# Kernel optimization log

Hardware: AMD Instinct MI355X
Metric: run time of the kernel (lower is better)

The kernel has to match this reference:

```python
import jax, jax.numpy as jnp
import numpy as np
import math

DIM = 512
HEADS = 8
DH = DIM // HEADS
B, C, H, W = 2, 512, 48, 48


def setup_inputs() -> dict:
    key = jax.random.key(0)
    k1, k2, k3, k4 = jax.random.split(key, 4)
    x = jax.random.normal(k1, (B, C, H, W), dtype=jnp.float32)
    # torch Linear weights: [out_features, in_features]
    w_qkv = jax.random.normal(k2, (3 * DIM, DIM), dtype=jnp.float32) * (DIM ** -0.5)
    w_out = jax.random.normal(k3, (DIM, DIM), dtype=jnp.float32) * (DIM ** -0.5)
    b_out = jax.random.normal(k4, (DIM,), dtype=jnp.float32) * 0.01
    wavelength = jnp.asarray(0.1, dtype=jnp.float32)
    return {"x": x, "w_qkv": w_qkv, "w_out": w_out, "b_out": b_out, "wavelength": wavelength}


def reference(x, w_qkv, w_out, b_out, wavelength):
    b, c, h, w = x.shape
    n = h * w
    scale = DH ** -0.5

    x_flat = x.reshape(b, c, n).transpose(0, 2, 1)  # [B, N, C]
    qkv = jnp.einsum('bnc,dc->bnd', x_flat, w_qkv)   # [B, N, 3*DIM]
    q, k, v = jnp.split(qkv, 3, axis=-1)

    def to_heads(t):
        return t.reshape(b, n, HEADS, DH).transpose(0, 2, 1, 3)  # [B, h, N, dh]

    q, k, v = to_heads(q), to_heads(k), to_heads(v)

    dots = jnp.einsum('bhid,bhjd->bhij', q, k) * scale  # [B, h, N, N]

    # Fresnel interference bias over spatial positions
    yy, xx = jnp.meshgrid(jnp.arange(h), jnp.arange(w), indexing='ij')
    positions = jnp.stack([yy, xx], axis=-1).astype(jnp.float32).reshape(-1, 2)  # [N, 2]
    pos_diff = positions[None, :, :] - positions[:, None, :]  # [N, N, 2]
    distances = jnp.sqrt(jnp.sum(pos_diff ** 2, axis=-1) + 1e-8)  # [N, N]
    phase = 2.0 * math.pi * distances / (jnp.abs(wavelength) * h + 1e-6)
    interference = jnp.cos(phase)

    dots = dots + interference[None, None, :, :] * 0.1
    attn = jax.nn.softmax(dots, axis=-1)
    out = jnp.einsum('bhij,bhjd->bhid', attn, v)  # [B, h, N, dh]
    out = out.transpose(0, 2, 1, 3).reshape(b, n, HEADS * DH)  # [B, N, DIM]
    out = jnp.einsum('bnd,od->bno', out, w_out) + b_out
    return out.transpose(0, 2, 1).reshape(b, c, h, w)
```

## Files before the change

### kernel.cpp

```cpp
#include <hip/hip_runtime.h>
#include <math.h>

#define BB 2
#define CC 512
#define NN 2304
#define NH 8
#define DD 512
#define D3 1536
#define WIDTH 48
#define C1 0.18033688f

#define KSPLIT 3
#define KTILES 12
#define NTBL 213

typedef _Float16 h8 __attribute__((ext_vector_type(8)));
typedef _Float16 h4 __attribute__((ext_vector_type(4)));
typedef _Float16 h2 __attribute__((ext_vector_type(2)));
typedef float f4 __attribute__((ext_vector_type(4)));

__device__ __forceinline__ void gload16(const void* g, void* s) {
  __builtin_amdgcn_global_load_lds(
      (const __attribute__((address_space(1))) unsigned int*)g,
      (__attribute__((address_space(3))) unsigned int*)s, 16, 0, 0);
}

__global__ __launch_bounds__(256) void prep_k(
    const float* __restrict__ x, const float* __restrict__ wq,
    const float* __restrict__ wo, const float* __restrict__ wavp,
    _Float16* __restrict__ xt, _Float16* __restrict__ wqh,
    _Float16* __restrict__ woh, _Float16* __restrict__ btf)
{
  __shared__ float Ls[32][33];
  const int t = threadIdx.x;
  const int e = blockIdx.x;

  if (e < 2304) {
    const int n0 = (e % 72) * 32;
    const int c0 = ((e / 72) % 16) * 32;
    const int b  = e / 1152;
#pragma unroll
    for (int p = 0; p < 4; ++p) {
      const int cl = (t >> 5) + p * 8, nl = t & 31;
      Ls[cl][nl] = x[((size_t)b * CC + c0 + cl) * NN + n0 + nl];
    }
    __syncthreads();
#pragma unroll
    for (int p = 0; p < 2; ++p) {
      const int nl = (t >> 4) + p * 16, cl = (t & 15) * 2;
      h2 v = {(_Float16)Ls[cl][nl], (_Float16)Ls[cl + 1][nl]};
      *(h2*)(xt + ((size_t)b * NN + n0 + nl) * CC + c0 + cl) = v;
    }
  } else if (e < 3328) {
    const int idx = (e - 2304) * 256 + t;
    const int NQ = (D3 * CC) / 4;
    if (idx < NQ) {
      float4 v = *(const float4*)(wq + (size_t)idx * 4);
      h4 o = {(_Float16)v.x, (_Float16)v.y, (_Float16)v.z, (_Float16)v.w};
      *(h4*)(wqh + (size_t)idx * 4) = o;
    } else {
      const int j = idx - NQ;
      float4 v = *(const float4*)(wo + (size_t)j * 4);
      h4 o = {(_Float16)v.x, (_Float16)v.y, (_Float16)v.z, (_Float16)v.w};
      *(h4*)(woh + (size_t)j * 4) = o;
    }
  } else {
    const int tbl = (e - 3328) * 2 + (t >> 7);
    if (tbl < NTBL) {
      const int tid = t & 127;
      const int dD = tbl / 3, qm = tbl % 3;
      const int qt0 = qm + 36;
      const int kt0 = qt0 - (dD - 35);
      const int w = tid >> 6, quad = (tid >> 4) & 3, l15 = tid & 15;
      const float pc = 6.283185307179586f / (fabsf(wavp[0]) * (float)WIDTH + 1e-6f);
      _Float16* o = btf + ((size_t)tbl * 128 + tid) * 32;
#pragma unroll
      for (int g = 0; g < 4; ++g) {
        h8 v;
#pragma unroll
        for (int el = 0; el < 8; ++el) {
          const int j = g * 8 + el;
          const int nt = j >> 4, mt = (j >> 2) & 3, r = j & 3;
          const int q = qt0 * 64 + w * 32 + nt * 16 + l15;
          const int k = kt0 * 64 + mt * 16 + quad * 4 + r;
          const float dy = (float)(q / WIDTH) - (float)(k / WIDTH);
          const float dx = (float)(q % WIDTH) - (float)(k % WIDTH);
          const float dist = sqrtf(dy * dy + dx * dx + 1e-8f);
          v[el] = (_Float16)(0.1f * __cosf(dist * pc) * 1.44269504f);
        }
        *(h8*)(o + g * 8) = v;
      }
    }
  }
}

__global__ __launch_bounds__(256) void qkv_gemm_k(
    const _Float16* __restrict__ xt, const _Float16* __restrict__ wqh,
    _Float16* __restrict__ qb, _Float16* __restrict__ kb,
    _Float16* __restrict__ vb)
{
  __shared__ _Float16 Xs[128][32];
  __shared__ _Float16 Ws[128][32];
  const int t = threadIdx.x;
  const int lane = t & 63, w = t >> 6;
  const int l15 = lane & 15, quad = lane >> 4;
  const int wm = w & 1, wn = w >> 1;
  const int n0 = blockIdx.x * 128;
  const int d0 = blockIdx.y * 128;
  const int b  = blockIdx.z;
  const bool isv = (d0 >= 2 * DD);
  const _Float16* xb = xt + (size_t)b * NN * CC;

  const int srow = lane >> 2, scol = (lane & 3) * 8;

  f4 acc[4][4];
#pragma unroll
  for (int mt = 0; mt < 4; ++mt)
#pragma unroll
    for (int nt = 0; nt < 4; ++nt) acc[mt][nt] = (f4)(0.f);

  for (int c0 = 0; c0 < CC; c0 += 32) {
#pragma unroll
    for (int r = 0; r < 2; ++r) {
      const int ci = w + r * 4;
      const int row = ci * 16 + srow;
      gload16(xb + (size_t)(n0 + row) * CC + c0 + scol, &Xs[0][0] + ci * 512);
      gload16(wqh + (size_t)(d0 + row) * CC + c0 + scol, &Ws[0][0] + ci * 512);
    }
    __syncthreads();

    h8 wfr[4], xfr[4];
#pragma unroll
    for (int mt = 0; mt < 4; ++mt)
      wfr[mt] = *(const h8*)&Ws[wm * 64 + mt * 16 + l15][quad * 8];
#pragma unroll
    for (int nt = 0; nt < 4; ++nt)
      xfr[nt] = *(const h8*)&Xs[wn * 64 + nt * 16 + l15][quad * 8];

    if (!isv) {
#pragma unroll
      for (int mt = 0; mt < 4; ++mt)
#pragma unroll
        for (int nt = 0; nt < 4; ++nt)
          acc[mt][nt] = __builtin_amdgcn_mfma_f32_16x16x32_f16(
              wfr[mt], xfr[nt], acc[mt][nt], 0, 0, 0);
    } else {
#pragma unroll
      for (int mt = 0; mt < 4; ++mt)
#pragma unroll
        for (int nt = 0; nt < 4; ++nt)
          acc[mt][nt] = __builtin_amdgcn_mfma_f32_16x16x32_f16(
              xfr[nt], wfr[mt], acc[mt][nt], 0, 0, 0);
    }
    __syncthreads();
  }

  if (!isv) {
    const int which = d0 >> 9;
    _Float16* buf = which == 0 ? qb : kb;
    const int h = ((d0 & 511) >> 6) + wm;
#pragma unroll
    for (int mt = 0; mt < 4; ++mt) {
      const int dh = mt * 16 + quad * 4;
#pragma unroll
      for (int nt = 0; nt < 4; ++nt) {
        const int token = n0 + wn * 64 + nt * 16 + l15;
        h4 o = {(_Float16)acc[mt][nt][0], (_Float16)acc[mt][nt][1],
                (_Float16)acc[mt][nt][2], (_Float16)acc[mt][nt][3]};
        *(h4*)(buf + (((size_t)b * NH + h) * NN + token) * 64 + dh) = o;
      }
    }
  } else {
    const int h = ((d0 - 2 * DD) >> 6) + wm;
#pragma unroll
    for (int mt = 0; mt < 4; ++mt) {
      const int dh = mt * 16 + l15;
#pragma unroll
      for (int nt = 0; nt < 4; ++nt) {
        const int token = n0 + wn * 64 + nt * 16 + quad * 4;
        h4 o = {(_Float16)acc[mt][nt][0], (_Float16)acc[mt][nt][1],
                (_Float16)acc[mt][nt][2], (_Float16)acc[mt][nt][3]};
        *(h4*)(vb + (((size_t)b * NH + h) * 64 + dh) * NN + token) = o;
      }
    }
  }
}

__global__ __launch_bounds__(128, 4) void attn_k(
    const _Float16* __restrict__ qb, const _Float16* __restrict__ kb,
    const _Float16* __restrict__ vb, const _Float16* __restrict__ btf,
    _Float16* __restrict__ op, float* __restrict__ lp)
{
  __shared__ _Float16 Ks[64][72];
  __shared__ _Float16 Vs[64][72];

  const int t    = threadIdx.x;
  const int lane = t & 63;
  const int w    = t >> 6;
  const int l15  = lane & 15;
  const int quad = lane >> 4;
  const int qtile = blockIdx.x / KSPLIT;
  const int kq    = blockIdx.x % KSPLIT;
  const int n0 = qtile * 64;
  const int h  = blockIdx.y;
  const int b  = blockIdx.z;
  const size_t base = ((size_t)b * NH + h) * NN * 64;
  const _Float16* qp = qb + base;
  const _Float16* kp = kb + base;
  const _Float16* vp = vb + base;

  h8 qf[2][2];
#pragma unroll
  for (int nt = 0; nt < 2; ++nt)
#pragma unroll
    for (int ks = 0; ks < 2; ++ks)
      qf[nt][ks] = *(const h8*)(qp + (size_t)(n0 + w * 32 + nt * 16 + l15) * 64 +
                                ks * 32 + quad * 8);

  f4 oc[4][2];
#pragma unroll
  for (int mt = 0; mt < 4; ++mt)
#pragma unroll
    for (int nt = 0; nt < 2; ++nt) oc[mt][nt] = (f4)(0.f);
  float lac[2][2] = {};

  const int ktg0 = kq * KTILES;
  const _Float16* bp =
      btf + ((size_t)((qtile - ktg0 + 35) * 3 + qtile % 3) * 128 + t) * 32;

  for (int kt = 0; kt < KTILES; ++kt) {
    const int k0 = (ktg0 + kt) * 64;
    h8 kr[4], vr[4], bfr[4];
#pragma unroll
    for (int r = 0; r < 4; ++r) {
      const int c = t + r * 128;
      const int row = c >> 3, off = (c & 7) * 8;
      kr[r] = *(const h8*)(kp + (size_t)(k0 + row) * 64 + off);
      vr[r] = *(const h8*)(vp + (size_t)row * NN + k0 + off);
      bfr[r] = *(const h8*)(bp + r * 8);
    }
    bp -= 3 * 128 * 32;
    __syncthreads();
#pragma unroll
    for (int r = 0; r < 4; ++r) {
      const int c = t + r * 128;
      const int row = c >> 3, off = (c & 7) * 8;
      *(h8*)&Ks[row][off] = kr[r];
      *(h8*)&Vs[row][off] = vr[r];
    }
    __syncthreads();

    f4 st[4][2];
#pragma unroll
    for (int mt = 0; mt < 4; ++mt)
#pragma unroll
      for (int nt = 0; nt < 2; ++nt) st[mt][nt] = (f4)(0.f);
#pragma unroll
    for (int ks = 0; ks < 2; ++ks) {
#pragma unroll
      for (int mt = 0; mt < 4; ++mt) {
        h8 kf = *(const h8*)&Ks[mt * 16 + l15][ks * 32 + quad * 8];
#pragma unroll
        for (int nt = 0; nt < 2; ++nt)
          st[mt][nt] = __builtin_amdgcn_mfma_f32_16x16x32_f16(
              kf, qf[nt][ks], st[mt][nt], 0, 0, 0);
      }
    }

    __syncthreads();

#pragma unroll
    for (int nt = 0; nt < 2; ++nt) {
      const int q = w * 32 + nt * 16 + l15;
#pragma unroll
      for (int mt = 0; mt < 4; ++mt) {
        const int jb = nt * 16 + mt * 4;
        const float b0 = (float)bfr[jb >> 3][(jb & 7) + 0];
        const float b1 = (float)bfr[jb >> 3][(jb & 7) + 1];
        const float b2 = (float)bfr[jb >> 3][(jb & 7) + 2];
        const float b3 = (float)bfr[jb >> 3][(jb & 7) + 3];
        const float p0 = __builtin_exp2f(st[mt][nt][0] * C1 + b0);
        const float p1 = __builtin_exp2f(st[mt][nt][1] * C1 + b1);
        const float p2 = __builtin_exp2f(st[mt][nt][2] * C1 + b2);
        const float p3 = __builtin_exp2f(st[mt][nt][3] * C1 + b3);
        lac[nt][0] += p0 + p1;
        lac[nt][1] += p2 + p3;
        const auto plo = __builtin_amdgcn_cvt_pkrtz(p0, p1);
        const auto phi = __builtin_amdgcn_cvt_pkrtz(p2, p3);
        h4 pk = {(_Float16)plo[0], (_Float16)plo[1],
                 (_Float16)phi[0], (_Float16)phi[1]};
        *(h4*)&Ks[q][mt * 16 + quad * 4] = pk;
      }
    }

#pragma unroll
    for (int ks = 0; ks < 2; ++ks) {
      h8 pf[2];
#pragma unroll
      for (int nt = 0; nt < 2; ++nt)
        pf[nt] = *(const h8*)&Ks[w * 32 + nt * 16 + l15][ks * 32 + quad * 8];
#pragma unroll
      for (int mt = 0; mt < 4; ++mt) {
        h8 vf = *(const h8*)&Vs[mt * 16 + l15][ks * 32 + quad * 8];
#pragma unroll
        for (int nt = 0; nt < 2; ++nt)
          oc[mt][nt] = __builtin_amdgcn_mfma_f32_16x16x32_f16(
              vf, pf[nt], oc[mt][nt], 0, 0, 0);
      }
    }
  }

#pragma unroll
  for (int nt = 0; nt < 2; ++nt) {
    float l = lac[nt][0] + lac[nt][1];
    l += __shfl_xor(l, 16);
    l += __shfl_xor(l, 32);
    const float inv = 1.f / l;
    const int qi = n0 + w * 32 + nt * 16 + l15;
    _Float16* od = op + (size_t)kq * BB * NN * DD +
                   ((size_t)b * NN + qi) * DD + h * 64;
#pragma unroll
    for (int mt = 0; mt < 4; ++mt) {
      const int dh = mt * 16 + quad * 4;
      h4 o = {(_Float16)(oc[mt][nt][0] * inv), (_Float16)(oc[mt][nt][1] * inv),
              (_Float16)(oc[mt][nt][2] * inv), (_Float16)(oc[mt][nt][3] * inv)};
      *(h4*)(od + dh) = o;
    }
    if (quad == 0)
      lp[(size_t)kq * BB * NH * NN + ((size_t)b * NH + h) * NN + qi] = l;
  }
}

__global__ __launch_bounds__(256) void comb_k(
    const _Float16* __restrict__ op, const float* __restrict__ lp,
    _Float16* __restrict__ ho)
{
  const int idx = blockIdx.x * 256 + threadIdx.x;
  const int d8 = idx & 63;
  const int bn = idx >> 6;
  const int n = bn % NN, b = bn / NN;
  const int h = d8 >> 3;
  const size_t SL = (size_t)BB * NH * NN;
  const size_t SO = (size_t)BB * NN * DD;
  const size_t li = ((size_t)b * NH + h) * NN + n;
  const float l0 = lp[li];
  const float l1 = lp[SL + li];
  const float l2 = lp[2 * SL + li];
  const float inv = 1.f / (l0 + l1 + l2);
  const float w0 = l0 * inv, w1 = l1 * inv, w2 = l2 * inv;
  h8 o0 = *(const h8*)(op + (size_t)bn * DD + d8 * 8);
  h8 o1 = *(const h8*)(op + SO + (size_t)bn * DD + d8 * 8);
  h8 o2 = *(const h8*)(op + 2 * SO + (size_t)bn * DD + d8 * 8);
  h8 r;
#pragma unroll
  for (int i = 0; i < 8; ++i)
    r[i] = (_Float16)((float)o0[i] * w0 + (float)o1[i] * w1 + (float)o2[i] * w2);
  *(h8*)(ho + (size_t)bn * DD + d8 * 8) = r;
}

__global__ __launch_bounds__(64) void out_gemm_k(
    const _Float16* __restrict__ ho, const _Float16* __restrict__ woh,
    const float* __restrict__ bias, float* __restrict__ out)
{
  __shared__ _Float16 Hs[64][32];
  __shared__ _Float16 Ws2[64][32];
  const int t = threadIdx.x;
  const int l15 = t & 15, quad = t >> 4;
  const int n0 = blockIdx.x * 64;
  const int o0 = blockIdx.y * 64;
  const int b  = blockIdx.z;
  const int srow = t >> 2, scol = (t & 3) * 8;

  f4 acc[4][4];
#pragma unroll
  for (int mt = 0; mt < 4; ++mt)
#pragma unroll
    for (int nt = 0; nt < 4; ++nt) acc[mt][nt] = (f4)(0.f);

  for (int c0 = 0; c0 < DD; c0 += 32) {
#pragma unroll
    for (int ci = 0; ci < 4; ++ci) {
      const int row = ci * 16 + srow;
      gload16(ho + ((size_t)b * NN + n0 + row) * DD + c0 + scol,
              &Hs[0][0] + ci * 512);
      gload16(woh + (size_t)(o0 + row) * DD + c0 + scol,
              &Ws2[0][0] + ci * 512);
    }
    __syncthreads();
    h8 hf[4], wf[4];
#pragma unroll
    for (int mt = 0; mt < 4; ++mt)
      hf[mt] = *(const h8*)&Hs[mt * 16 + l15][quad * 8];
#pragma unroll
    for (int nt = 0; nt < 4; ++nt)
      wf[nt] = *(const h8*)&Ws2[nt * 16 + l15][quad * 8];
#pragma unroll
    for (int mt = 0; mt < 4; ++mt)
#pragma unroll
      for (int nt = 0; nt < 4; ++nt)
        acc[mt][nt] = __builtin_amdgcn_mfma_f32_16x16x32_f16(
            hf[mt], wf[nt], acc[mt][nt], 0, 0, 0);
    __syncthreads();
  }

#pragma unroll
  for (int nt = 0; nt < 4; ++nt) {
    const int o = o0 + nt * 16 + l15;
    const float bv = bias[o];
#pragma unroll
    for (int mt = 0; mt < 4; ++mt) {
      const int token = n0 + mt * 16 + quad * 4;
      float4 v = {acc[mt][nt][0] + bv, acc[mt][nt][1] + bv,
                  acc[mt][nt][2] + bv, acc[mt][nt][3] + bv};
      *(float4*)(out + ((size_t)b * DD + o) * NN + token) = v;
    }
  }
}

extern "C" void kernel_launch(void* const* d_in, const int* in_sizes, int n_in,
                              void* d_out, int out_size, void* d_ws, size_t ws_size,
                              hipStream_t stream)
{
  (void)in_sizes; (void)n_in; (void)out_size; (void)ws_size;
  const float* x     = (const float*)d_in[0];
  const float* w_qkv = (const float*)d_in[1];
  const float* w_out = (const float*)d_in[2];
  const float* b_out = (const float*)d_in[3];
  const float* wav   = (const float*)d_in[4];
  float* out = (float*)d_out;

  const size_t SZ  = (size_t)BB * NH * NN * 64;
  const size_t BTF = (size_t)NTBL * 128 * 32;

  _Float16* qb  = (_Float16*)d_ws;
  _Float16* kb  = qb + SZ;
  _Float16* vb  = kb + SZ;
  _Float16* btf = vb + SZ;
  _Float16* op  = btf + BTF;
  float*    lpf = (float*)(op + 3 * SZ);
  _Float16* woh = (_Float16*)(lpf + 3 * (size_t)BB * NH * NN);
  _Float16* ho  = qb;
  _Float16* xt  = op;
  _Float16* wqh = op + SZ;

  prep_k    <<<dim3(2304 + 1024 + 107), 256, 0, stream>>>(x, w_qkv, w_out, wav,
                                                          xt, wqh, woh, btf);
  qkv_gemm_k<<<dim3(NN / 128, D3 / 128, BB), 256, 0, stream>>>(xt, wqh, qb, kb, vb);
  attn_k    <<<dim3(NN / 64 * KSPLIT, NH, BB), 128, 0, stream>>>(qb, kb, vb, btf, op, lpf);
  comb_k    <<<dim3((BB * NN * 64) / 256), 256, 0, stream>>>(op, lpf, ho);
  out_gemm_k<<<dim3(NN / 64, DD / 64, BB), 64, 0, stream>>>(ho, woh, b_out, out);
}
```

Baseline: 173.5 us.

## Seed attention accumulators with fp32 bias, fold Q scale, reduce key split

The Fresnel bias table is now stored in fp32 in the MFMA accumulator layout. It is loaded directly as the initial value of the QK^T accumulators, and the softmax scale is folded into Q in the QKV GEMM epilogue. This removes the per-element bias conversion and the multiply-add before exp2 in the attention inner loop. The key-dimension split drops from 3 to 2 partitions with 18 tiles each, and the combine kernel and workspace layout are updated to match, which cuts partial-output traffic. The cost is twice the bias-table bytes read per tile and fewer attention blocks in flight.

```diff
diff --git a/kernel.cpp b/kernel.cpp
--- a/kernel.cpp
+++ b/kernel.cpp
@@ -10,8 +10,8 @@
 #define WIDTH 48
 #define C1 0.18033688f
 
-#define KSPLIT 3
-#define KTILES 12
+#define KSPLIT 2
+#define KTILES 18
 #define NTBL 213
 
 typedef _Float16 h8 __attribute__((ext_vector_type(8)));
@@ -29,7 +29,7 @@
     const float* __restrict__ x, const float* __restrict__ wq,
     const float* __restrict__ wo, const float* __restrict__ wavp,
     _Float16* __restrict__ xt, _Float16* __restrict__ wqh,
-    _Float16* __restrict__ woh, _Float16* __restrict__ btf)
+    _Float16* __restrict__ woh, float* __restrict__ btf)
 {
   __shared__ float Ls[32][33];
   const int t = threadIdx.x;
@@ -73,22 +73,22 @@
       const int kt0 = qt0 - (dD - 35);
       const int w = tid >> 6, quad = (tid >> 4) & 3, l15 = tid & 15;
       const float pc = 6.283185307179586f / (fabsf(wavp[0]) * (float)WIDTH + 1e-6f);
-      _Float16* o = btf + ((size_t)tbl * 128 + tid) * 32;
-#pragma unroll
-      for (int g = 0; g < 4; ++g) {
-        h8 v;
-#pragma unroll
-        for (int el = 0; el < 8; ++el) {
-          const int j = g * 8 + el;
+      float* o = btf + ((size_t)tbl * 128 + tid) * 32;
+#pragma unroll
+      for (int g = 0; g < 8; ++g) {
+        f4 v;
+#pragma unroll
+        for (int el = 0; el < 4; ++el) {
+          const int j = g * 4 + el;
           const int nt = j >> 4, mt = (j >> 2) & 3, r = j & 3;
           const int q = qt0 * 64 + w * 32 + nt * 16 + l15;
           const int k = kt0 * 64 + mt * 16 + quad * 4 + r;
           const float dy = (float)(q / WIDTH) - (float)(k / WIDTH);
           const float dx = (float)(q % WIDTH) - (float)(k % WIDTH);
           const float dist = sqrtf(dy * dy + dx * dx + 1e-8f);
-          v[el] = (_Float16)(0.1f * __cosf(dist * pc) * 1.44269504f);
+          v[el] = 0.1f * __cosf(dist * pc) * 1.44269504f;
         }
-        *(h8*)(o + g * 8) = v;
+        *(f4*)(o + g * 4) = v;
       }
     }
   }
@@ -158,6 +158,7 @@
   if (!isv) {
     const int which = d0 >> 9;
     _Float16* buf = which == 0 ? qb : kb;
+    const float qs = (which == 0) ? C1 : 1.0f;
     const int h = ((d0 & 511) >> 6) + wm;
 #pragma unroll
     for (int mt = 0; mt < 4; ++mt) {
@@ -165,8 +166,8 @@
 #pragma unroll
       for (int nt = 0; nt < 4; ++nt) {
         const int token = n0 + wn * 64 + nt * 16 + l15;
-        h4 o = {(_Float16)acc[mt][nt][0], (_Float16)acc[mt][nt][1],
-                (_Float16)acc[mt][nt][2], (_Float16)acc[mt][nt][3]};
+        h4 o = {(_Float16)(acc[mt][nt][0] * qs), (_Float16)(acc[mt][nt][1] * qs),
+                (_Float16)(acc[mt][nt][2] * qs), (_Float16)(acc[mt][nt][3] * qs)};
         *(h4*)(buf + (((size_t)b * NH + h) * NN + token) * 64 + dh) = o;
       }
     }
@@ -188,7 +189,7 @@
 
 __global__ __launch_bounds__(128, 4) void attn_k(
     const _Float16* __restrict__ qb, const _Float16* __restrict__ kb,
-    const _Float16* __restrict__ vb, const _Float16* __restrict__ btf,
+    const _Float16* __restrict__ vb, const float* __restrict__ btf,
     _Float16* __restrict__ op, float* __restrict__ lp)
 {
   __shared__ _Float16 Ks[64][72];
@@ -199,8 +200,8 @@
   const int w    = t >> 6;
   const int l15  = lane & 15;
   const int quad = lane >> 4;
-  const int qtile = blockIdx.x / KSPLIT;
-  const int kq    = blockIdx.x % KSPLIT;
+  const int qtile = blockIdx.x >> 1;
+  const int kq    = blockIdx.x & 1;
   const int n0 = qtile * 64;
   const int h  = blockIdx.y;
   const int b  = blockIdx.z;
@@ -225,20 +226,22 @@
   float lac[2][2] = {};
 
   const int ktg0 = kq * KTILES;
-  const _Float16* bp =
+  const float* bp =
       btf + ((size_t)((qtile - ktg0 + 35) * 3 + qtile % 3) * 128 + t) * 32;
 
   for (int kt = 0; kt < KTILES; ++kt) {
     const int k0 = (ktg0 + kt) * 64;
-    h8 kr[4], vr[4], bfr[4];
+    h8 kr[4], vr[4];
+    f4 bfr[8];
 #pragma unroll
     for (int r = 0; r < 4; ++r) {
       const int c = t + r * 128;
       const int row = c >> 3, off = (c & 7) * 8;
       kr[r] = *(const h8*)(kp + (size_t)(k0 + row) * 64 + off);
       vr[r] = *(const h8*)(vp + (size_t)row * NN + k0 + off);
-      bfr[r] = *(const h8*)(bp + r * 8);
-    }
+    }
+#pragma unroll
+    for (int r = 0; r < 8; ++r) bfr[r] = *(const f4*)(bp + r * 4);
     bp -= 3 * 128 * 32;
     __syncthreads();
 #pragma unroll
@@ -254,7 +257,7 @@
 #pragma unroll
     for (int mt = 0; mt < 4; ++mt)
 #pragma unroll
-      for (int nt = 0; nt < 2; ++nt) st[mt][nt] = (f4)(0.f);
+      for (int nt = 0; nt < 2; ++nt) st[mt][nt] = bfr[nt * 4 + mt];
 #pragma unroll
     for (int ks = 0; ks < 2; ++ks) {
 #pragma unroll
@@ -274,15 +277,10 @@
       const int q = w * 32 + nt * 16 + l15;
 #pragma unroll
       for (int mt = 0; mt < 4; ++mt) {
-        const int jb = nt * 16 + mt * 4;
-        const float b0 = (float)bfr[jb >> 3][(jb & 7) + 0];
-        const float b1 = (float)bfr[jb >> 3][(jb & 7) + 1];
-        const float b2 = (float)bfr[jb >> 3][(jb & 7) + 2];
-        const float b3 = (float)bfr[jb >> 3][(jb & 7) + 3];
-        const float p0 = __builtin_exp2f(st[mt][nt][0] * C1 + b0);
-        const float p1 = __builtin_exp2f(st[mt][nt][1] * C1 + b1);
-        const float p2 = __builtin_exp2f(st[mt][nt][2] * C1 + b2);
-        const float p3 = __builtin_exp2f(st[mt][nt][3] * C1 + b3);
+        const float p0 = __builtin_exp2f(st[mt][nt][0]);
+        const float p1 = __builtin_exp2f(st[mt][nt][1]);
+        const float p2 = __builtin_exp2f(st[mt][nt][2]);
+        const float p3 = __builtin_exp2f(st[mt][nt][3]);
         lac[nt][0] += p0 + p1;
         lac[nt][1] += p2 + p3;
         const auto plo = __builtin_amdgcn_cvt_pkrtz(p0, p1);
@@ -345,16 +343,14 @@
   const size_t li = ((size_t)b * NH + h) * NN + n;
   const float l0 = lp[li];
   const float l1 = lp[SL + li];
-  const float l2 = lp[2 * SL + li];
-  const float inv = 1.f / (l0 + l1 + l2);
-  const float w0 = l0 * inv, w1 = l1 * inv, w2 = l2 * inv;
+  const float inv = 1.f / (l0 + l1);
+  const float w0 = l0 * inv, w1 = l1 * inv;
   h8 o0 = *(const h8*)(op + (size_t)bn * DD + d8 * 8);
   h8 o1 = *(const h8*)(op + SO + (size_t)bn * DD + d8 * 8);
-  h8 o2 = *(const h8*)(op + 2 * SO + (size_t)bn * DD + d8 * 8);
   h8 r;
 #pragma unroll
   for (int i = 0; i < 8; ++i)
-    r[i] = (_Float16)((float)o0[i] * w0 + (float)o1[i] * w1 + (float)o2[i] * w2);
+    r[i] = (_Float16)((float)o0[i] * w0 + (float)o1[i] * w1);
   *(h8*)(ho + (size_t)bn * DD + d8 * 8) = r;
 }
 
@@ -435,10 +431,10 @@
   _Float16* qb  = (_Float16*)d_ws;
   _Float16* kb  = qb + SZ;
   _Float16* vb  = kb + SZ;
-  _Float16* btf = vb + SZ;
-  _Float16* op  = btf + BTF;
-  float*    lpf = (float*)(op + 3 * SZ);
-  _Float16* woh = (_Float16*)(lpf + 3 * (size_t)BB * NH * NN);
+  float*    btf = (float*)(vb + SZ);
+  _Float16* op  = (_Float16*)(btf + BTF);
+  float*    lpf = (float*)(op + 2 * SZ);
+  _Float16* woh = (_Float16*)(lpf + 2 * (size_t)BB * NH * NN);
   _Float16* ho  = qb;
   _Float16* xt  = op;
   _Float16* wqh = op + SZ;
```

Result: slower. 210.7 us (+21.4%).
